# Performance work log

Measured on AMD Instinct MI355X. Metric: run time of the kernel, lower is better.

## Reference

```python
import jax, jax.numpy as jnp
import numpy as np

# config (mirrors init_kwargs)
R = 1.0           # ball-query radius
K = 32            # ball-query neighbors
SPATIAL_STRIDE = 4
TKS = 3           # temporal kernel size (odd)
TPAD = (1, 1)     # replicate temporal padding
HEADS = 8
DIM_HEAD = 64
DIM = 512
MLP = 2048
DEPTH = 2
LN_EPS = 1e-5


def fps(xyz, m):
    # CUDA-style furthest point sampling, starts at index 0. xyz: [N,3] -> [m] int32
    N = xyz.shape[0]
    def body(carry, _):
        dists, last = carry
        d = jnp.sum((xyz - xyz[last]) ** 2, axis=-1)
        dists = jnp.minimum(dists, d)
        nxt = jnp.argmax(dists).astype(jnp.int32)
        return (dists, nxt), nxt
    init = (jnp.full((N,), 1e10, xyz.dtype), jnp.int32(0))
    _, idxs = jax.lax.scan(body, init, None, length=m - 1)
    return jnp.concatenate([jnp.zeros((1,), jnp.int32), idxs])


def ball_query(neighbor_xyz, anchor_xyz):
    # first K neighbor indices within radius R (pad with first found, 0 if none)
    N = neighbor_xyz.shape[0]
    d2 = jnp.sum((anchor_xyz[:, None, :] - neighbor_xyz[None, :, :]) ** 2, -1)  # [M,N]
    cand = jnp.where(d2 < R * R, jnp.arange(N, dtype=jnp.int32)[None, :], N)
    firstk = jnp.sort(cand, axis=-1)[:, :K]
    first = firstk[:, :1]
    idx = jnp.where(firstk >= N, first, firstk)
    return jnp.where(idx >= N, 0, idx).astype(jnp.int32)


def layer_norm(x, g, b):
    mu = jnp.mean(x, -1, keepdims=True)
    var = jnp.var(x, -1, keepdims=True)
    return (x - mu) * jax.lax.rsqrt(var + LN_EPS) * g + b


def p4dconv(xyzs, Wd):
    # tube embedding: FPS anchors + ball-query grouping + 1x1 conv on (dx,dy,dz,dt)
    B, T, N, _ = xyzs.shape
    pad = jnp.concatenate([xyzs[:, :1]] * TPAD[0] + [xyzs] + [xyzs[:, -1:]] * TPAD[1], axis=1)
    Lp = pad.shape[1]
    m = N // SPATIAL_STRIDE
    half = TKS // 2
    new_xyzs, new_feats = [], []
    for t in range(half, Lp - half, 1):  # temporal_stride = 1
        frame = pad[:, t]                                  # [B,N,3]
        aidx = jax.vmap(lambda x: fps(x, m))(frame)        # [B,m]
        anchor = jax.vmap(lambda f, ix: f[ix])(frame, aidx)  # [B,m,3]
        feats_t = []
        for i in range(t - half, t + half + 1):
            nb = pad[:, i]                                 # [B,N,3]
            idx = jax.vmap(ball_query)(nb, anchor)         # [B,m,K]
            grouped = jax.vmap(lambda n, ix: n[ix])(nb, idx)  # [B,m,K,3]
            disp = grouped - anchor[:, :, None, :]
            tdisp = jnp.full((B, m, K, 1), float(i - t), disp.dtype)
            d4 = jnp.concatenate([disp, tdisp], -1)        # [B,m,K,4]
            f = jnp.einsum('bmkf,cf->bmkc', d4, Wd)        # 1x1 conv, no bias/BN/act
            feats_t.append(jnp.max(f, axis=2))             # spatial max pool
        new_feats.append(jnp.max(jnp.stack(feats_t, 1), axis=1))  # temporal max pool
        new_xyzs.append(anchor)
    return jnp.stack(new_xyzs, 1), jnp.stack(new_feats, 1)  # [B,L,m,3], [B,L,m,C]


def attention(xyzs, feats, Wqkv, Wsp, Wout, bout, g, b):
    B, L, n, C = feats.shape
    M = L * n
    x = layer_norm(feats, g, b)
    qkv = jnp.einsum('blnc,ec->blne', x, Wqkv).reshape(B, M, 3, HEADS, DIM_HEAD)
    q, k, v = [jnp.transpose(qkv[:, :, j], (0, 2, 1, 3)) for j in range(3)]  # [B,h,M,d]
    dots = jnp.einsum('bhid,bhjd->bhij', q, k) * (DIM_HEAD ** -0.5)
    attn = jax.nn.softmax(dots, axis=-1)
    out_v = jnp.einsum('bhij,bhjd->bhid', attn, v)
    xyz_f = xyzs.reshape(B, M, 3)
    delta = xyz_f[:, None, :, :] - xyz_f[:, :, None, :]      # [B,i,j,3] = xyz_j - xyz_i
    wdelta = jnp.einsum('bhij,bijc->bhic', attn, delta)      # attn-weighted displacement
    disp_f = jnp.einsum('bhic,dc->bhid', wdelta, Wsp)        # spatial_op Linear(3->d)
    out = out_v + disp_f
    out = jnp.transpose(out, (0, 2, 1, 3)).reshape(B, M, HEADS * DIM_HEAD)
    out = jax.nn.gelu(out @ Wout.T + bout, approximate=False)
    return out.reshape(B, L, n, C) + feats


def feed_forward(x, g, b, W1, b1, W2, b2):
    h = layer_norm(x, g, b)
    h = jax.nn.gelu(h @ W1.T + b1, approximate=False)
    return h @ W2.T + b2 + x


def setup_inputs() -> dict:
    key = jax.random.key(0)
    ks = jax.random.split(key, 12)
    s = 0.02
    inner = HEADS * DIM_HEAD
    return {
        'xyzs': jax.random.normal(ks[0], (2, 4, 1024, 3), jnp.float32),
        'Wd': jax.random.normal(ks[1], (DIM, 4), jnp.float32) * s,
        'Wqkv': jax.random.normal(ks[2], (DEPTH, 3 * inner, DIM), jnp.float32) * s,
        'Wsp': jax.random.normal(ks[3], (DEPTH, DIM_HEAD, 3), jnp.float32) * s,
        'Wout': jax.random.normal(ks[4], (DEPTH, DIM, inner), jnp.float32) * s,
        'bout': jnp.zeros((DEPTH, DIM), jnp.float32),
        'ln1_g': jnp.ones((DEPTH, DIM), jnp.float32),
        'ln1_b': jnp.zeros((DEPTH, DIM), jnp.float32),
        'Wff1': jax.random.normal(ks[5], (DEPTH, MLP, DIM), jnp.float32) * s,
        'bff1': jnp.zeros((DEPTH, MLP), jnp.float32),
        'Wff2': jax.random.normal(ks[6], (DEPTH, DIM, MLP), jnp.float32) * s,
        'bff2': jnp.zeros((DEPTH, DIM), jnp.float32),
        'ln2_g': jnp.ones((DEPTH, DIM), jnp.float32),
        'ln2_b': jnp.zeros((DEPTH, DIM), jnp.float32),
    }


def reference(xyzs, Wd, Wqkv, Wsp, Wout, bout, ln1_g, ln1_b, Wff1, bff1, Wff2, bff2, ln2_g, ln2_b):
    new_xyzs, feats = p4dconv(xyzs, Wd)   # [B,L,m,3], [B,L,m,DIM]
    feats = jax.nn.relu(feats)            # emb_relu after tube embedding
    for i in range(DEPTH):
        feats = attention(new_xyzs, feats, Wqkv[i], Wsp[i], Wout[i], bout[i], ln1_g[i], ln1_b[i])
        feats = feed_forward(feats, ln2_g[i], ln2_b[i], Wff1[i], bff1[i], Wff2[i], bff2[i])
    return feats
```

## Files before the change

kernel.cpp:

```cpp
#include <hip/hip_runtime.h>
#include <math.h>
#include <stdint.h>


typedef __bf16 bf16_t;
typedef __bf16 bf16x8 __attribute__((ext_vector_type(8)));
typedef __bf16 bf16x4 __attribute__((ext_vector_type(4)));
typedef float f32x4 __attribute__((ext_vector_type(4)));

__device__ __forceinline__ void async16(const bf16_t* g, bf16_t* l) {
  __builtin_amdgcn_global_load_lds(
      (const __attribute__((address_space(1))) void*)g,
      (__attribute__((address_space(3))) void*)l, 16, 0, 0);
}

__device__ __forceinline__ float wave_max_dpp(float v) {
  int a = __float_as_int(v);
  int t;
  t = __builtin_amdgcn_update_dpp(a, a, 0x111, 0xf, 0xf, false);
  a = __float_as_int(fmaxf(__int_as_float(a), __int_as_float(t)));
  t = __builtin_amdgcn_update_dpp(a, a, 0x112, 0xf, 0xf, false);
  a = __float_as_int(fmaxf(__int_as_float(a), __int_as_float(t)));
  t = __builtin_amdgcn_update_dpp(a, a, 0x114, 0xf, 0xf, false);
  a = __float_as_int(fmaxf(__int_as_float(a), __int_as_float(t)));
  t = __builtin_amdgcn_update_dpp(a, a, 0x118, 0xf, 0xf, false);
  a = __float_as_int(fmaxf(__int_as_float(a), __int_as_float(t)));
  t = __builtin_amdgcn_update_dpp(a, a, 0x142, 0xf, 0xf, false);
  a = __float_as_int(fmaxf(__int_as_float(a), __int_as_float(t)));
  t = __builtin_amdgcn_update_dpp(a, a, 0x143, 0xf, 0xf, false);
  a = __float_as_int(fmaxf(__int_as_float(a), __int_as_float(t)));
  return __int_as_float(a);
}

template <int CTRL>
__device__ __forceinline__ void tourney(unsigned long long& kv, float& x,
                                        float& y, float& z) {
  uint32_t lo = (uint32_t)kv, hi = (uint32_t)(kv >> 32);
  uint32_t lo2 =
      (uint32_t)__builtin_amdgcn_update_dpp((int)lo, (int)lo, CTRL, 0xf, 0xf, false);
  uint32_t hi2 =
      (uint32_t)__builtin_amdgcn_update_dpp((int)hi, (int)hi, CTRL, 0xf, 0xf, false);
  float x2 = __int_as_float(__builtin_amdgcn_update_dpp(
      __float_as_int(x), __float_as_int(x), CTRL, 0xf, 0xf, false));
  float y2 = __int_as_float(__builtin_amdgcn_update_dpp(
      __float_as_int(y), __float_as_int(y), CTRL, 0xf, 0xf, false));
  float z2 = __int_as_float(__builtin_amdgcn_update_dpp(
      __float_as_int(z), __float_as_int(z), CTRL, 0xf, 0xf, false));
  unsigned long long other = ((unsigned long long)hi2 << 32) | lo2;
  bool take = other > kv;
  kv = take ? other : kv;
  x = take ? x2 : x;
  y = take ? y2 : y;
  z = take ? z2 : z;
}

__global__ __launch_bounds__(512) void fps_cvt_kernel(
    const float* __restrict__ xyzs, float* __restrict__ anchors,
    const float* __restrict__ s0, bf16_t* __restrict__ d0,
    const float* __restrict__ s1, bf16_t* __restrict__ d1,
    const float* __restrict__ s2, bf16_t* __restrict__ d2,
    const float* __restrict__ s3, bf16_t* __restrict__ d3) {
  int bid = blockIdx.x;
  int tid = threadIdx.x;
  if (bid >= 8) {
    int idx = (bid - 8) * 512 + tid;
    const float* s; bf16_t* d; int off;
    if (idx < 393216) { s = s0; d = d0; off = idx; }
    else if (idx < 524288) { s = s1; d = d1; off = idx - 393216; }
    else if (idx < 1048576) { s = s2; d = d2; off = idx - 524288; }
    else { s = s3; d = d3; off = idx - 1048576; }
    float4 v = ((const float4*)s)[off];
    bf16x4 o = {(bf16_t)v.x, (bf16_t)v.y, (bf16_t)v.z, (bf16_t)v.w};
    ((bf16x4*)d)[off] = o;
    return;
  }
  int to = bid & 3, b = bid >> 2;
  const float* fr = xyzs + (size_t)(b * 4 + to) * 1024 * 3;
  float* an = anchors + (size_t)(b * 4 + to) * 256 * 3;
  __shared__ __align__(16) float4 cand[2][8];
  __shared__ __align__(16) unsigned long long keys[2][8];
  int w = tid >> 6, lane = tid & 63;
  float px[2], py[2], pz[2], dist[2];
#pragma unroll
  for (int r = 0; r < 2; ++r) {
    int i = r * 512 + tid;
    px[r] = fr[i * 3 + 0]; py[r] = fr[i * 3 + 1]; pz[r] = fr[i * 3 + 2];
    dist[r] = 1e10f;
  }
  float cx = fr[0], cy = fr[1], cz = fr[2];
  if (tid == 0) { an[0] = cx; an[1] = cy; an[2] = cz; }
  for (int s = 1; s < 256; ++s) {
    int par = s & 1;
#pragma unroll
    for (int r = 0; r < 2; ++r) {
      float dx = px[r] - cx, dy = py[r] - cy, dz = pz[r] - cz;
      float d = fmaf(dx, dx, fmaf(dy, dy, dz * dz));
      dist[r] = fminf(dist[r], d);
    }
    float mloc = fmaxf(dist[0], dist[1]);
    float wmax = wave_max_dpp(mloc);
    float smax = __int_as_float(__builtin_amdgcn_readlane(__float_as_int(wmax), 63));
    unsigned int cidx = 0xFFFFFFFFu;
#pragma unroll
    for (int r = 1; r >= 0; --r) {
      unsigned long long m = __ballot(dist[r] == smax);
      unsigned int tz = (unsigned int)__builtin_ctzll(m | 0x8000000000000000ull);
      unsigned int candi = (unsigned int)(r * 512 + w * 64) + tz;
      cidx = m ? candi : cidx;
    }
    unsigned long long key =
        ((unsigned long long)__float_as_uint(smax) << 32) |
        (unsigned long long)(~cidx);
    int wl = (int)(cidx & 63u), rsel = (int)(cidx >> 9);
    if (lane == wl) {
      cand[par][w] = make_float4(rsel ? px[1] : px[0], rsel ? py[1] : py[0],
                                 rsel ? pz[1] : pz[0], 0.0f);
    }
    if (lane == 0) keys[par][w] = key;
    __syncthreads();
    unsigned long long kv = keys[par][lane & 7];
    float4 cd = cand[par][lane & 7];
    float tx = cd.x, ty = cd.y, tz2 = cd.z;
    tourney<0xB1>(kv, tx, ty, tz2);
    tourney<0x4E>(kv, tx, ty, tz2);
    tourney<0x124>(kv, tx, ty, tz2);
    cx = tx; cy = ty; cz = tz2;
    if (tid == 0) { an[s * 3 + 0] = cx; an[s * 3 + 1] = cy; an[s * 3 + 2] = cz; }
  }
}

__global__ __launch_bounds__(192) void conv_kernel(
    const float* __restrict__ xyzs, const float* __restrict__ anchors,
    const float* __restrict__ Wd, float* __restrict__ feats) {
  int bid = blockIdx.x;
  int j = bid & 255, to = (bid >> 8) & 3, b = bid >> 10;
  __shared__ float disp[96][4];
  __shared__ int idxbuf[3][32];
  const float* an = anchors + (size_t)((b * 4 + to) * 256 + j) * 3;
  float ax = an[0], ay = an[1], az = an[2];
  int w = threadIdx.x >> 6, lane = threadIdx.x & 63;
  int src = to + w - 1; src = src < 0 ? 0 : (src > 3 ? 3 : src);
  const float* nb = xyzs + (size_t)(b * 4 + src) * 1024 * 3;
  int cnt = 0;
  for (int ch = 0; ch < 16; ++ch) {
    if (cnt >= 32) break;
    int i = ch * 64 + lane;
    float dx = ax - nb[i * 3], dy = ay - nb[i * 3 + 1], dz = az - nb[i * 3 + 2];
    float d2 = dx * dx + dy * dy + dz * dz;
    bool in = d2 < 1.0f;
    unsigned long long mask = __ballot(in);
    if (in) {
      int pos = cnt + (int)__popcll(mask & ((1ull << lane) - 1ull));
      if (pos < 32) idxbuf[w][pos] = i;
    }
    cnt += (int)__popcll(mask);
  }
  if (cnt > 32) cnt = 32;
  if (lane >= cnt && lane < 32) idxbuf[w][lane] = (cnt > 0) ? idxbuf[w][0] : 0;
  if (lane < 32) {
    int ni = idxbuf[w][lane];
    int row = w * 32 + lane;
    disp[row][0] = nb[ni * 3 + 0] - ax;
    disp[row][1] = nb[ni * 3 + 1] - ay;
    disp[row][2] = nb[ni * 3 + 2] - az;
    disp[row][3] = (float)(w - 1);
  }
  __syncthreads();
  float* fout = feats + ((size_t)(b * 1024) + to * 256 + j) * 512;
  for (int c = threadIdx.x; c < 512; c += 192) {
    const float* wr = Wd + c * 4;
    float w0 = wr[0], w1 = wr[1], w2 = wr[2], w3 = wr[3];
    float mx = -1e30f;
#pragma unroll 8
    for (int nn = 0; nn < 96; ++nn) {
      float v = disp[nn][0] * w0 + disp[nn][1] * w1 + disp[nn][2] * w2 + disp[nn][3] * w3;
      mx = fmaxf(mx, v);
    }
    fout[c] = fmaxf(mx, 0.0f);
  }
}

__global__ __launch_bounds__(256) void ln_kernel(
    const float* __restrict__ x, const float* __restrict__ g,
    const float* __restrict__ bt, bf16_t* __restrict__ y) {
  int row = blockIdx.x;
  int tid = threadIdx.x;
  const float* xr = x + (size_t)row * 512;
  float v0 = xr[tid], v1 = xr[tid + 256];
  float s = v0 + v1;
#pragma unroll
  for (int off = 32; off >= 1; off >>= 1) s += __shfl_xor(s, off, 64);
  __shared__ float red1[4], red2[4];
  int w = tid >> 6, lane = tid & 63;
  if (lane == 0) red1[w] = s;
  __syncthreads();
  float mu = (red1[0] + red1[1] + red1[2] + red1[3]) * (1.0f / 512.0f);
  float d0 = v0 - mu, d1 = v1 - mu;
  float q = d0 * d0 + d1 * d1;
#pragma unroll
  for (int off = 32; off >= 1; off >>= 1) q += __shfl_xor(q, off, 64);
  if (lane == 0) red2[w] = q;
  __syncthreads();
  float var = (red2[0] + red2[1] + red2[2] + red2[3]) * (1.0f / 512.0f);
  float rs = rsqrtf(var + 1e-5f);
  bf16_t* yr = y + (size_t)row * 512;
  yr[tid] = (bf16_t)(d0 * rs * g[tid] + bt[tid]);
  yr[tid + 256] = (bf16_t)(d1 * rs * g[tid + 256] + bt[tid + 256]);
}

template <int BM, int BN, bool GELU, bool BIAS, bool RES, bool OUTBF>
__global__ __launch_bounds__(256) void gemm_bf16(
    const bf16_t* __restrict__ A, const bf16_t* __restrict__ W,
    const float* __restrict__ bias, const float* __restrict__ res,
    void* __restrict__ Cout, int Mn, int Nn, int Kn) {
  constexpr int BK = 64;
  constexpr int WM = BM / 2, WN = BN / 2;
  constexpr int MT = WM / 16, NT = WN / 16;
  constexpr int AIT = (BM * BK / 8) / 256;
  constexpr int BIT = (BN * BK / 8) / 256;
  __shared__ __align__(16) bf16_t As[BM * BK];
  __shared__ __align__(16) bf16_t Bs[BN * BK];
  int tid = threadIdx.x;
  int w = tid >> 6, lane = tid & 63;
  int wr = w >> 1, wc = w & 1;
  int m0 = blockIdx.y * BM, n0 = blockIdx.x * BN;
  int l15 = lane & 15, quad = lane >> 4;
  f32x4 acc[MT][NT] = {};

  const int a_fo = (wr * WM + l15) * BK + quad * 8;
  const int b_fo = (wc * WN + l15) * BK + quad * 8;

  for (int k0 = 0; k0 < Kn; k0 += BK) {
    __syncthreads();
#pragma unroll
    for (int i = 0; i < AIT; ++i) {
      int chunk = i * 256 + tid;
      int row = chunk >> 3, c8 = chunk & 7;
      async16(A + ((size_t)(m0 + row) * Kn + k0 + c8 * 8), As + chunk * 8);
    }
#pragma unroll
    for (int i = 0; i < BIT; ++i) {
      int chunk = i * 256 + tid;
      int row = chunk >> 3, c8 = chunk & 7;
      async16(W + ((size_t)(n0 + row) * Kn + k0 + c8 * 8), Bs + chunk * 8);
    }
    __syncthreads();
#pragma unroll
    for (int ks = 0; ks < 2; ++ks) {
      bf16x8 aF[MT], bF[NT];
#pragma unroll
      for (int mt = 0; mt < MT; ++mt)
        aF[mt] = *(const bf16x8*)&As[a_fo + mt * 16 * BK + ks * 32];
#pragma unroll
      for (int nt = 0; nt < NT; ++nt)
        bF[nt] = *(const bf16x8*)&Bs[b_fo + nt * 16 * BK + ks * 32];
#pragma unroll
      for (int mt = 0; mt < MT; ++mt)
#pragma unroll
        for (int nt = 0; nt < NT; ++nt)
          acc[mt][nt] = __builtin_amdgcn_mfma_f32_16x16x32_bf16(
              aF[mt], bF[nt], acc[mt][nt], 0, 0, 0);
    }
  }
  int rbase = quad * 4;
#pragma unroll
  for (int mt = 0; mt < MT; ++mt) {
#pragma unroll
    for (int reg = 0; reg < 4; ++reg) {
      int r = m0 + wr * WM + mt * 16 + rbase + reg;
      size_t roff = (size_t)r * Nn;
#pragma unroll
      for (int nt = 0; nt < NT; ++nt) {
        int c = n0 + wc * WN + nt * 16 + l15;
        float v = acc[mt][nt][reg];
        if (BIAS) v += bias[c];
        if (GELU) v = v * 0.5f * (1.0f + erff(v * 0.7071067811865475f));
        if (RES) v += res[roff + c];
        if (OUTBF) ((bf16_t*)Cout)[roff + c] = (bf16_t)v;
        else ((float*)Cout)[roff + c] = v;
      }
    }
  }
}

__global__ __launch_bounds__(256) void attn_kernel(
    const bf16_t* __restrict__ qkv, const float* __restrict__ xyzf,
    const float* __restrict__ Wsp, bf16_t* __restrict__ outp) {
  int bid = blockIdx.x;
  int qt = bid & 15, h = (bid >> 4) & 7, b = bid >> 7;
  int tid = threadIdx.x;
  int w = tid >> 6, lane = tid & 63;
  int l15 = lane & 15, quad = lane >> 4;

  __shared__ __align__(16) bf16_t Kb[2][64 * 64];
  __shared__ __align__(16) bf16_t Vt[2][64 * 72];
  __shared__ __align__(16) bf16_t Ps[4][16 * 72];
  __shared__ __align__(16) float4 Xs[2][64];

  const size_t tokbase = (size_t)b * 1024;
  int qbase = qt * 64 + w * 16;

  bf16x8 aQ[2];
  {
    const bf16_t* qp = qkv + (tokbase + qbase + l15) * 1536 + h * 64 + quad * 8;
    aQ[0] = *(const bf16x8*)(qp);
    aQ[1] = *(const bf16x8*)(qp + 32);
  }

  f32x4 oacc[4] = {};
  float lr[4] = {}, pxr[4] = {}, pyr[4] = {}, pzr[4] = {};

  auto stage = [&](int ch, int buf) {
    int j0 = ch * 64;
    int r0 = tid >> 3, seg = tid & 7;
    const bf16_t* g0 = qkv + (tokbase + j0 + r0) * 1536 + 512 + h * 64 + seg * 8;
    async16(g0, Kb[buf] + tid * 8);
    const bf16_t* g1 = qkv + (tokbase + j0 + 32 + r0) * 1536 + 512 + h * 64 + seg * 8;
    async16(g1, Kb[buf] + 2048 + tid * 8);
#pragma unroll
    for (int t = 0; t < 4; ++t) {
      int task = t * 256 + tid;
      int rp = task >> 5, c2 = task & 31;
      const uint32_t* vsrc = (const uint32_t*)(qkv + (tokbase + j0 + 2 * rp) * 1536 +
                                               1024 + h * 64 + 2 * c2);
      uint32_t a = vsrc[0];
      uint32_t bq = vsrc[768];
      uint32_t wlo = (a & 0xffffu) | (bq << 16);
      uint32_t whi = (a >> 16) | (bq & 0xffff0000u);
      uint32_t* vd = (uint32_t*)Vt[buf];
      vd[c2 * 72 + rp] = wlo;
      vd[c2 * 72 + 36 + rp] = whi;
    }
    if (tid < 64) {
      const float* xp = xyzf + (tokbase + j0 + tid) * 3;
      Xs[buf][tid] = make_float4(xp[0], xp[1], xp[2], 0.0f);
    }
  };

  stage(0, 0);
  for (int ch = 0; ch < 16; ++ch) {
    int cur = ch & 1;
    __syncthreads();
    if (ch + 1 < 16) stage(ch + 1, cur ^ 1);
    f32x4 sacc[4] = {};
#pragma unroll
    for (int ks = 0; ks < 2; ++ks)
#pragma unroll
      for (int nt = 0; nt < 4; ++nt) {
        bf16x8 bK = *(const bf16x8*)&Kb[cur][(nt * 16 + l15) * 64 + ks * 32 + quad * 8];
        sacc[nt] = __builtin_amdgcn_mfma_f32_16x16x32_bf16(aQ[ks], bK, sacc[nt], 0, 0, 0);
      }
#pragma unroll
    for (int nt = 0; nt < 4; ++nt) {
      float4 xk = Xs[cur][nt * 16 + l15];
#pragma unroll
      for (int reg = 0; reg < 4; ++reg) {
        float p = __expf(sacc[nt][reg] * 0.125f);
        bf16_t pb = (bf16_t)p;
        float pf = (float)pb;
        Ps[w][(quad * 4 + reg) * 72 + nt * 16 + l15] = pb;
        lr[reg] += pf;
        pxr[reg] = fmaf(pf, xk.x, pxr[reg]);
        pyr[reg] = fmaf(pf, xk.y, pyr[reg]);
        pzr[reg] = fmaf(pf, xk.z, pzr[reg]);
      }
    }
    bf16x8 aP[2];
    aP[0] = *(const bf16x8*)&Ps[w][l15 * 72 + quad * 8];
    aP[1] = *(const bf16x8*)&Ps[w][l15 * 72 + 32 + quad * 8];
#pragma unroll
    for (int ks = 0; ks < 2; ++ks)
#pragma unroll
      for (int ct = 0; ct < 4; ++ct) {
        bf16x8 bV = *(const bf16x8*)&Vt[cur][(ct * 16 + l15) * 72 + ks * 32 + quad * 8];
        oacc[ct] = __builtin_amdgcn_mfma_f32_16x16x32_bf16(aP[ks], bV, oacc[ct], 0, 0, 0);
      }
  }
#pragma unroll
  for (int reg = 0; reg < 4; ++reg) {
#pragma unroll
    for (int off = 1; off <= 8; off <<= 1) {
      lr[reg] += __shfl_xor(lr[reg], off, 64);
      pxr[reg] += __shfl_xor(pxr[reg], off, 64);
      pyr[reg] += __shfl_xor(pyr[reg], off, 64);
      pzr[reg] += __shfl_xor(pzr[reg], off, 64);
    }
  }
#pragma unroll
  for (int reg = 0; reg < 4; ++reg) {
    size_t tok = tokbase + qbase + quad * 4 + reg;
    float inv = 1.0f / lr[reg];
    const float* xqp = xyzf + tok * 3;
    float wd0 = pxr[reg] * inv - xqp[0];
    float wd1 = pyr[reg] * inv - xqp[1];
    float wd2 = pzr[reg] * inv - xqp[2];
#pragma unroll
    for (int ct = 0; ct < 4; ++ct) {
      int c = ct * 16 + l15;
      const float* wr = Wsp + c * 3;
      float dv = wd0 * wr[0] + wd1 * wr[1] + wd2 * wr[2];
      outp[tok * 512 + h * 64 + c] = (bf16_t)(oacc[ct][reg] * inv + dv);
    }
  }
}

extern "C" void kernel_launch(void* const* d_in, const int* in_sizes, int n_in,
                              void* d_out, int out_size, void* d_ws, size_t ws_size,
                              hipStream_t stream) {
  const float* xyzs = (const float*)d_in[0];
  const float* Wd   = (const float*)d_in[1];
  const float* Wqkv = (const float*)d_in[2];
  const float* Wsp  = (const float*)d_in[3];
  const float* Wout = (const float*)d_in[4];
  const float* bout = (const float*)d_in[5];
  const float* ln1g = (const float*)d_in[6];
  const float* ln1b = (const float*)d_in[7];
  const float* Wff1 = (const float*)d_in[8];
  const float* bff1 = (const float*)d_in[9];
  const float* Wff2 = (const float*)d_in[10];
  const float* bff2 = (const float*)d_in[11];
  const float* ln2g = (const float*)d_in[12];
  const float* ln2b = (const float*)d_in[13];
  float* out = (float*)d_out;

  float* ws = (float*)d_ws;
  float* anchors = ws;
  float* featsA  = ws + 8192;
  float* featsB  = featsA + 1048576;
  float* big     = featsB + 1048576;
  bf16_t* bigb   = (bf16_t*)big;
  bf16_t* xlnb   = (bf16_t*)(big + 3145728);
  bf16_t* attob  = xlnb + 1048576;
  bf16_t* wq_b   = attob + 1048576;
  bf16_t* wo_b   = wq_b + 1572864;
  bf16_t* w1_b   = wo_b + 524288;
  bf16_t* w2_b   = w1_b + 2097152;

  fps_cvt_kernel<<<3080, 512, 0, stream>>>(xyzs, anchors, Wqkv, wq_b, Wout, wo_b,
                                           Wff1, w1_b, Wff2, w2_b);
  conv_kernel<<<2048, 192, 0, stream>>>(xyzs, anchors, Wd, featsA);

  for (int dep = 0; dep < 2; ++dep) {
    ln_kernel<<<2048, 256, 0, stream>>>(featsA, ln1g + dep * 512, ln1b + dep * 512, xlnb);
    gemm_bf16<64, 128, false, false, false, true><<<dim3(12, 32), 256, 0, stream>>>(
        xlnb, wq_b + (size_t)dep * 786432, nullptr, nullptr, bigb, 2048, 1536, 512);
    attn_kernel<<<256, 256, 0, stream>>>(bigb, anchors, Wsp + dep * 192, attob);
    gemm_bf16<32, 64, true, true, true, false><<<dim3(8, 64), 256, 0, stream>>>(
        attob, wo_b + (size_t)dep * 262144, bout + dep * 512, featsA, featsB,
        2048, 512, 512);
    ln_kernel<<<2048, 256, 0, stream>>>(featsB, ln2g + dep * 512, ln2b + dep * 512, xlnb);
    gemm_bf16<64, 128, true, true, false, true><<<dim3(16, 32), 256, 0, stream>>>(
        xlnb, w1_b + (size_t)dep * 1048576, bff1 + dep * 2048, nullptr, bigb,
        2048, 2048, 512);
    float* dst = (dep == 1) ? out : featsA;
    gemm_bf16<32, 64, false, true, true, false><<<dim3(8, 64), 256, 0, stream>>>(
        bigb, w2_b + (size_t)dep * 1048576, bff2 + dep * 512, featsB, dst,
        2048, 512, 2048);
  }
}
```

Baseline: 466.5 us.

## Fuse first LayerNorm into tube-conv kernel and move weight conversion there

```diff
diff --git a/kernel.cpp b/kernel.cpp
--- a/kernel.cpp
+++ b/kernel.cpp
@@ -54,26 +54,10 @@
   z = take ? z2 : z;
 }
 
-__global__ __launch_bounds__(512) void fps_cvt_kernel(
-    const float* __restrict__ xyzs, float* __restrict__ anchors,
-    const float* __restrict__ s0, bf16_t* __restrict__ d0,
-    const float* __restrict__ s1, bf16_t* __restrict__ d1,
-    const float* __restrict__ s2, bf16_t* __restrict__ d2,
-    const float* __restrict__ s3, bf16_t* __restrict__ d3) {
+__global__ __launch_bounds__(512) void fps_kernel(const float* __restrict__ xyzs,
+                                                  float* __restrict__ anchors) {
   int bid = blockIdx.x;
   int tid = threadIdx.x;
-  if (bid >= 8) {
-    int idx = (bid - 8) * 512 + tid;
-    const float* s; bf16_t* d; int off;
-    if (idx < 393216) { s = s0; d = d0; off = idx; }
-    else if (idx < 524288) { s = s1; d = d1; off = idx - 393216; }
-    else if (idx < 1048576) { s = s2; d = d2; off = idx - 524288; }
-    else { s = s3; d = d3; off = idx - 1048576; }
-    float4 v = ((const float4*)s)[off];
-    bf16x4 o = {(bf16_t)v.x, (bf16_t)v.y, (bf16_t)v.z, (bf16_t)v.w};
-    ((bf16x4*)d)[off] = o;
-    return;
-  }
   int to = bid & 3, b = bid >> 2;
   const float* fr = xyzs + (size_t)(b * 4 + to) * 1024 * 3;
   float* an = anchors + (size_t)(b * 4 + to) * 256 * 3;
@@ -129,55 +113,102 @@
   }
 }
 
-__global__ __launch_bounds__(192) void conv_kernel(
+__global__ __launch_bounds__(256) void conv_cvt_kernel(
     const float* __restrict__ xyzs, const float* __restrict__ anchors,
-    const float* __restrict__ Wd, float* __restrict__ feats) {
+    const float* __restrict__ Wd, float* __restrict__ feats,
+    bf16_t* __restrict__ xln0, const float* __restrict__ g,
+    const float* __restrict__ bt,
+    const float* __restrict__ s0, bf16_t* __restrict__ d0,
+    const float* __restrict__ s1, bf16_t* __restrict__ d1,
+    const float* __restrict__ s2, bf16_t* __restrict__ d2,
+    const float* __restrict__ s3, bf16_t* __restrict__ d3) {
   int bid = blockIdx.x;
+  int tid = threadIdx.x;
+  if (bid >= 2048) {
+    int base = (bid - 2048) * 256 + tid;
+#pragma unroll
+    for (int t = 0; t < 3; ++t) {
+      int idx = base + t * 524288;
+      const float* s; bf16_t* d; int off;
+      if (idx < 393216) { s = s0; d = d0; off = idx; }
+      else if (idx < 524288) { s = s1; d = d1; off = idx - 393216; }
+      else if (idx < 1048576) { s = s2; d = d2; off = idx - 524288; }
+      else { s = s3; d = d3; off = idx - 1048576; }
+      float4 v = ((const float4*)s)[off];
+      bf16x4 o = {(bf16_t)v.x, (bf16_t)v.y, (bf16_t)v.z, (bf16_t)v.w};
+      ((bf16x4*)d)[off] = o;
+    }
+    return;
+  }
   int j = bid & 255, to = (bid >> 8) & 3, b = bid >> 10;
   __shared__ float disp[96][4];
   __shared__ int idxbuf[3][32];
+  __shared__ float red1[4], red2[4];
   const float* an = anchors + (size_t)((b * 4 + to) * 256 + j) * 3;
   float ax = an[0], ay = an[1], az = an[2];
-  int w = threadIdx.x >> 6, lane = threadIdx.x & 63;
-  int src = to + w - 1; src = src < 0 ? 0 : (src > 3 ? 3 : src);
-  const float* nb = xyzs + (size_t)(b * 4 + src) * 1024 * 3;
-  int cnt = 0;
-  for (int ch = 0; ch < 16; ++ch) {
-    if (cnt >= 32) break;
-    int i = ch * 64 + lane;
-    float dx = ax - nb[i * 3], dy = ay - nb[i * 3 + 1], dz = az - nb[i * 3 + 2];
-    float d2 = dx * dx + dy * dy + dz * dz;
-    bool in = d2 < 1.0f;
-    unsigned long long mask = __ballot(in);
-    if (in) {
-      int pos = cnt + (int)__popcll(mask & ((1ull << lane) - 1ull));
-      if (pos < 32) idxbuf[w][pos] = i;
-    }
-    cnt += (int)__popcll(mask);
-  }
-  if (cnt > 32) cnt = 32;
-  if (lane >= cnt && lane < 32) idxbuf[w][lane] = (cnt > 0) ? idxbuf[w][0] : 0;
-  if (lane < 32) {
-    int ni = idxbuf[w][lane];
-    int row = w * 32 + lane;
-    disp[row][0] = nb[ni * 3 + 0] - ax;
-    disp[row][1] = nb[ni * 3 + 1] - ay;
-    disp[row][2] = nb[ni * 3 + 2] - az;
-    disp[row][3] = (float)(w - 1);
+  int w = tid >> 6, lane = tid & 63;
+  if (w < 3) {
+    int src = to + w - 1; src = src < 0 ? 0 : (src > 3 ? 3 : src);
+    const float* nb = xyzs + (size_t)(b * 4 + src) * 1024 * 3;
+    int cnt = 0;
+    for (int ch = 0; ch < 16; ++ch) {
+      if (cnt >= 32) break;
+      int i = ch * 64 + lane;
+      float dx = ax - nb[i * 3], dy = ay - nb[i * 3 + 1], dz = az - nb[i * 3 + 2];
+      float d2 = dx * dx + dy * dy + dz * dz;
+      bool in = d2 < 1.0f;
+      unsigned long long mask = __ballot(in);
+      if (in) {
+        int pos = cnt + (int)__popcll(mask & ((1ull << lane) - 1ull));
+        if (pos < 32) idxbuf[w][pos] = i;
+      }
+      cnt += (int)__popcll(mask);
+    }
+    if (cnt > 32) cnt = 32;
+    if (lane >= cnt && lane < 32) idxbuf[w][lane] = (cnt > 0) ? idxbuf[w][0] : 0;
+    if (lane < 32) {
+      int ni = idxbuf[w][lane];
+      int row = w * 32 + lane;
+      disp[row][0] = nb[ni * 3 + 0] - ax;
+      disp[row][1] = nb[ni * 3 + 1] - ay;
+      disp[row][2] = nb[ni * 3 + 2] - az;
+      disp[row][3] = (float)(w - 1);
+    }
   }
   __syncthreads();
-  float* fout = feats + ((size_t)(b * 1024) + to * 256 + j) * 512;
-  for (int c = threadIdx.x; c < 512; c += 192) {
-    const float* wr = Wd + c * 4;
-    float w0 = wr[0], w1 = wr[1], w2 = wr[2], w3 = wr[3];
-    float mx = -1e30f;
+  int row = (b * 1024) + to * 256 + j;
+  const float* wr0 = Wd + tid * 4;
+  const float* wr1 = Wd + (tid + 256) * 4;
+  float w00 = wr0[0], w01 = wr0[1], w02 = wr0[2], w03 = wr0[3];
+  float w10 = wr1[0], w11 = wr1[1], w12 = wr1[2], w13 = wr1[3];
+  float mx0 = -1e30f, mx1 = -1e30f;
 #pragma unroll 8
-    for (int nn = 0; nn < 96; ++nn) {
-      float v = disp[nn][0] * w0 + disp[nn][1] * w1 + disp[nn][2] * w2 + disp[nn][3] * w3;
-      mx = fmaxf(mx, v);
-    }
-    fout[c] = fmaxf(mx, 0.0f);
-  }
+  for (int nn = 0; nn < 96; ++nn) {
+    float a0 = disp[nn][0], a1 = disp[nn][1], a2 = disp[nn][2], a3 = disp[nn][3];
+    mx0 = fmaxf(mx0, a0 * w00 + a1 * w01 + a2 * w02 + a3 * w03);
+    mx1 = fmaxf(mx1, a0 * w10 + a1 * w11 + a2 * w12 + a3 * w13);
+  }
+  float v0 = fmaxf(mx0, 0.0f), v1 = fmaxf(mx1, 0.0f);
+  float* fout = feats + (size_t)row * 512;
+  fout[tid] = v0;
+  fout[tid + 256] = v1;
+  float s = v0 + v1;
+#pragma unroll
+  for (int off = 32; off >= 1; off >>= 1) s += __shfl_xor(s, off, 64);
+  if (lane == 0) red1[w] = s;
+  __syncthreads();
+  float mu = (red1[0] + red1[1] + red1[2] + red1[3]) * (1.0f / 512.0f);
+  float dd0 = v0 - mu, dd1 = v1 - mu;
+  float q = dd0 * dd0 + dd1 * dd1;
+#pragma unroll
+  for (int off = 32; off >= 1; off >>= 1) q += __shfl_xor(q, off, 64);
+  if (lane == 0) red2[w] = q;
+  __syncthreads();
+  float var = (red2[0] + red2[1] + red2[2] + red2[3]) * (1.0f / 512.0f);
+  float rs = rsqrtf(var + 1e-5f);
+  bf16_t* yr = xln0 + (size_t)row * 512;
+  yr[tid] = (bf16_t)(dd0 * rs * g[tid] + bt[tid]);
+  yr[tid + 256] = (bf16_t)(dd1 * rs * g[tid + 256] + bt[tid + 256]);
 }
 
 __global__ __launch_bounds__(256) void ln_kernel(
@@ -436,12 +467,14 @@
   bf16_t* w1_b   = wo_b + 524288;
   bf16_t* w2_b   = w1_b + 2097152;
 
-  fps_cvt_kernel<<<3080, 512, 0, stream>>>(xyzs, anchors, Wqkv, wq_b, Wout, wo_b,
-                                           Wff1, w1_b, Wff2, w2_b);
-  conv_kernel<<<2048, 192, 0, stream>>>(xyzs, anchors, Wd, featsA);
+  fps_kernel<<<8, 512, 0, stream>>>(xyzs, anchors);
+  conv_cvt_kernel<<<4096, 256, 0, stream>>>(
+      xyzs, anchors, Wd, featsA, xlnb, ln1g, ln1b,
+      Wqkv, wq_b, Wout, wo_b, Wff1, w1_b, Wff2, w2_b);
 
   for (int dep = 0; dep < 2; ++dep) {
-    ln_kernel<<<2048, 256, 0, stream>>>(featsA, ln1g + dep * 512, ln1b + dep * 512, xlnb);
+    if (dep == 1)
+      ln_kernel<<<2048, 256, 0, stream>>>(featsA, ln1g + 512, ln1b + 512, xlnb);
     gemm_bf16<64, 128, false, false, false, true><<<dim3(12, 32), 256, 0, stream>>>(
         xlnb, wq_b + (size_t)dep * 786432, nullptr, nullptr, bigb, 2048, 1536, 512);
     attn_kernel<<<256, 256, 0, stream>>>(bigb, anchors, Wsp + dep * 192, attob);
```

After: 440.8 us. 5.5% less time.
